# Kernel tuning notes

Measured on AMD Instinct MI355X. Metric: run time of the kernel, lower is better.

The kernel has to match this reference:

```python
import jax, jax.numpy as jnp
import numpy as np
from jax import lax

D_MODEL = 1024
N_HEADS = 8
D_HEAD = 64
D_INNER = N_HEADS * D_HEAD  # 512
B, T = 4, 4096
LN_EPS = 1e-5
NORM_EPS = 1e-12  # F.normalize default eps


def setup_inputs() -> dict:
    key = jax.random.key(0)
    ks = jax.random.split(key, 6)
    s_proj = (2.0 / (D_MODEL + D_INNER)) ** 0.5  # xavier_uniform-ish std
    x = jax.random.normal(ks[0], (B, T, D_MODEL), jnp.float32)
    Wq = jax.random.normal(ks[1], (D_MODEL, D_INNER), jnp.float32) * s_proj
    Wk = jax.random.normal(ks[2], (D_MODEL, D_INNER), jnp.float32) * s_proj
    Wv = jax.random.normal(ks[3], (D_MODEL, D_INNER), jnp.float32) * s_proj
    Wa = jax.random.normal(ks[4], (D_MODEL, D_INNER), jnp.float32) * s_proj
    ba = jnp.full((D_INNER,), 3.0, jnp.float32)  # nn.init.constant_(W_alpha.bias, 3.0)
    Wo = jax.random.normal(ks[5], (D_INNER, D_MODEL), jnp.float32) * s_proj
    gamma = jnp.ones((D_MODEL,), jnp.float32)
    beta = jnp.zeros((D_MODEL,), jnp.float32)
    return {"x": x, "Wq": Wq, "Wk": Wk, "Wv": Wv, "Wa": Wa, "ba": ba,
            "Wo": Wo, "gamma": gamma, "beta": beta}


def reference(x, Wq, Wk, Wv, Wa, ba, Wo, gamma, beta):
    Bx, Tx, _ = x.shape
    residual = x
    # LayerNorm
    mu = jnp.mean(x, axis=-1, keepdims=True)
    var = jnp.var(x, axis=-1, keepdims=True)
    xn = (x - mu) / jnp.sqrt(var + LN_EPS) * gamma + beta
    # Projections -> (B, T, H, d) -> time-major (T, B, H, d) for scan
    def heads(y):
        return jnp.moveaxis(y.reshape(Bx, Tx, N_HEADS, D_HEAD), 1, 0)
    q = heads(xn @ Wq)
    k = heads(xn @ Wk)
    v = heads(xn @ Wv)
    alpha = jax.nn.sigmoid(heads(xn @ Wa + ba))
    # F.normalize(k, dim=-1)
    knorm = jnp.linalg.norm(k, axis=-1, keepdims=True)
    k = k / jnp.maximum(knorm, NORM_EPS)

    # Recurrence: S_t = diag(a_t) S_{t-1} + k_t v_t^T ; o_t = S_t^T q_t
    def step(S, inp):
        q_t, k_t, v_t, a_t = inp  # each (B, H, d)
        S = a_t[..., None] * S + k_t[..., None] * v_t[..., None, :]  # (B,H,dk,dv)
        o_t = jnp.einsum('bhji,bhj->bhi', S, q_t)
        return S, o_t

    S0 = jnp.zeros((Bx, N_HEADS, D_HEAD, D_HEAD), x.dtype)
    _, outs = lax.scan(step, S0, (q, k, v, alpha))  # outs: (T, B, H, d)
    out = jnp.moveaxis(outs, 0, 1).reshape(Bx, Tx, D_INNER) @ Wo
    return out + residual
```

## Files before the change

### kernel.cpp

```cpp
#include <hip/hip_runtime.h>
#include <stdint.h>

#define NTOK   16384
#define DM     1024
#define DI     512
#define NH     8
#define DH     64
#define CHUNK  64
#define NCH    64
#define NBHC   2048

using short8 = __attribute__((ext_vector_type(8))) short;
using f32x4  = __attribute__((ext_vector_type(4))) float;

__device__ __forceinline__ unsigned short f2bf(float f) {
  union { float f; unsigned int u; } x; x.f = f;
  unsigned int u = x.u;
  return (unsigned short)((u + 0x7fffu + ((u >> 16) & 1u)) >> 16);
}
__device__ __forceinline__ float bf2f(unsigned short h) {
  union { unsigned int u; float f; } x; x.u = ((unsigned int)h) << 16; return x.f;
}

typedef const __attribute__((address_space(1))) void* gp1_t;
typedef __attribute__((address_space(3))) void* lp3_t;
__device__ __forceinline__ void gload_lds16(const void* g, void* l) {
  __builtin_amdgcn_global_load_lds((gp1_t)g, (lp3_t)l, 16, 0, 0);
}

__global__ __launch_bounds__(256) void init_kernel(const float* __restrict__ x,
                                                   const float* __restrict__ gamma,
                                                   const float* __restrict__ beta,
                                                   const float* __restrict__ Wq,
                                                   const float* __restrict__ Wk,
                                                   const float* __restrict__ Wv,
                                                   const float* __restrict__ Wa,
                                                   const float* __restrict__ Wo,
                                                   unsigned short* __restrict__ xn,
                                                   unsigned short* __restrict__ Wt,
                                                   unsigned short* __restrict__ Wot) {
  const int blk = blockIdx.x, tid = threadIdx.x;
  __shared__ float tile[32][33];
  __shared__ float rs_[4], rss_[4];
  if (blk < NTOK) {
    const int row = blk;
    float4 v = ((const float4*)(x + (long)row * DM))[tid];
    float s  = v.x + v.y + v.z + v.w;
    float ss = v.x * v.x + v.y * v.y + v.z * v.z + v.w * v.w;
    #pragma unroll
    for (int off = 32; off > 0; off >>= 1) { s += __shfl_down(s, off); ss += __shfl_down(ss, off); }
    int wave = tid >> 6, lane = tid & 63;
    if (lane == 0) { rs_[wave] = s; rss_[wave] = ss; }
    __syncthreads();
    s  = rs_[0] + rs_[1] + rs_[2] + rs_[3];
    ss = rss_[0] + rss_[1] + rss_[2] + rss_[3];
    float mu   = s * (1.f / DM);
    float var  = ss * (1.f / DM) - mu * mu;
    float rstd = rsqrtf(var + 1e-5f);
    int idx = tid * 4;
    float xv[4] = {v.x, v.y, v.z, v.w};
    unsigned short o[4];
    #pragma unroll
    for (int j = 0; j < 4; ++j) o[j] = f2bf((xv[j] - mu) * rstd * gamma[idx + j] + beta[idx + j]);
    uint2 pk; pk.x = (unsigned)o[0] | ((unsigned)o[1] << 16); pk.y = (unsigned)o[2] | ((unsigned)o[3] << 16);
    *(uint2*)(xn + (long)row * DM + idx) = pk;
  } else if (blk < NTOK + 2048) {
    const int id = blk - NTOK;
    const int z = id >> 9, r9 = id & 511;
    const float* in = (z == 0) ? Wq : (z == 1) ? Wk : (z == 2) ? Wv : Wa;
    unsigned short* o = Wt + (size_t)z * 512 * 1024;
    int bx = (r9 & 15) * 32, by = (r9 >> 4) * 32;
    int tx = tid & 31, ty = tid >> 5;
    #pragma unroll
    for (int r = ty; r < 32; r += 8) tile[r][tx] = in[(long)(by + r) * 512 + bx + tx];
    __syncthreads();
    #pragma unroll
    for (int r = ty; r < 32; r += 8) o[(long)(bx + r) * 1024 + by + tx] = f2bf(tile[tx][r]);
  } else {
    const int id = blk - NTOK - 2048;
    int bx = (id & 31) * 32, by = (id >> 5) * 32;
    int tx = tid & 31, ty = tid >> 5;
    #pragma unroll
    for (int r = ty; r < 32; r += 8) tile[r][tx] = Wo[(long)(by + r) * 1024 + bx + tx];
    __syncthreads();
    #pragma unroll
    for (int r = ty; r < 32; r += 8) Wot[(long)(bx + r) * 512 + by + tx] = f2bf(tile[tx][r]);
  }
}

#define EPSW 264
#define G4_TILE(T_, DOSTAGE_, WAITC_)                                         \
  {                                                                           \
    if (DOSTAGE_) {                                                           \
      const int s_ = (T_) + 3;                                                \
      unsigned short* sb_ = &sm[(s_ & 3) * 16384];                            \
      const long ko_ = (long)s_ * 32;                                         \
      gload_lds16(a0p + ko_, sb_ + dst);                                      \
      gload_lds16(a1p + ko_, sb_ + 4096 + dst);                               \
      gload_lds16(b0p + ko_, sb_ + 8192 + dst);                               \
      gload_lds16(b1p + ko_, sb_ + 12288 + dst);                              \
    }                                                                         \
    const unsigned short* cb_ = &sm[((T_) & 3) * 16384];                      \
    short8 av_[8], bv_[4];                                                    \
    _Pragma("unroll")                                                         \
    for (int mt = 0; mt < 8; ++mt) av_[mt] = *(const short8*)&cb_[aoff + mt * 512]; \
    _Pragma("unroll")                                                         \
    for (int nt = 0; nt < 4; ++nt) bv_[nt] = *(const short8*)&cb_[boff + nt * 512]; \
    __builtin_amdgcn_s_setprio(1);                                            \
    _Pragma("unroll")                                                         \
    for (int mt = 0; mt < 8; ++mt)                                            \
      _Pragma("unroll")                                                       \
      for (int nt = 0; nt < 4; ++nt)                                          \
        acc[mt][nt] = __builtin_amdgcn_mfma_f32_16x16x32_bf16(av_[mt], bv_[nt], acc[mt][nt], 0, 0, 0); \
    __builtin_amdgcn_s_setprio(0);                                            \
    asm volatile("s_waitcnt " WAITC_ ::: "memory");                           \
    __builtin_amdgcn_s_barrier();                                             \
    __builtin_amdgcn_sched_barrier(0);                                        \
  }

template <int MODE>
__global__ __launch_bounds__(512, 2) void gemm4s(const unsigned short* __restrict__ A,
                                                 const unsigned short* __restrict__ Bt,
                                                 unsigned short* __restrict__ Cb,
                                                 float* __restrict__ Cf,
                                                 const float* __restrict__ resid,
                                                 int M, int N, int K) {
  __shared__ __align__(16) unsigned short sm[65536];
  const int tid = threadIdx.x;
  const int wave = tid >> 6, lane = tid & 63;
  const int quad = lane >> 4, l16 = lane & 15;
  const int wm = wave >> 2, wn = wave & 3;

  const int nwg = gridDim.x;
  const int cpx = nwg >> 3;
  const int bid = blockIdx.x;
  const int swz = (bid & 7) * cpx + (bid >> 3);
  const int m0 = (swz & 63) * 256;
  const int n0 = (swz >> 6) * 256;

  const int r2 = tid >> 2;
  const int scol = ((tid & 3) * 8) ^ (((tid >> 3) & 3) * 8);
  const unsigned short* a0p = A + (long)(m0 + r2) * K + scol;
  const unsigned short* a1p = A + (long)(m0 + 128 + r2) * K + scol;
  const unsigned short* b0p = Bt + (long)(n0 + r2) * K + scol;
  const unsigned short* b1p = Bt + (long)(n0 + 128 + r2) * K + scol;
  const int dst = tid * 8;

  const int swzr = (quad * 8) ^ (((l16 >> 1) & 3) * 8);
  const int aoff = (wm * 128 + l16) * 32 + swzr;
  const int boff = 8192 + (wn * 64 + l16) * 32 + swzr;

  f32x4 acc[8][4];
  #pragma unroll
  for (int i = 0; i < 8; ++i)
    #pragma unroll
    for (int j = 0; j < 4; ++j) acc[i][j] = (f32x4){0.f, 0.f, 0.f, 0.f};

  const int NT = K >> 5;

  #pragma unroll
  for (int s = 0; s < 3; ++s) {
    unsigned short* sb = &sm[s * 16384];
    const long ko = (long)s * 32;
    gload_lds16(a0p + ko, sb + dst);
    gload_lds16(a1p + ko, sb + 4096 + dst);
    gload_lds16(b0p + ko, sb + 8192 + dst);
    gload_lds16(b1p + ko, sb + 12288 + dst);
  }
  asm volatile("s_waitcnt vmcnt(8)" ::: "memory");
  __builtin_amdgcn_s_barrier();
  __builtin_amdgcn_sched_barrier(0);

  int t = 0;
  for (; t < NT - 3; ++t) G4_TILE(t, true, "vmcnt(8)");
  G4_TILE(t, false, "vmcnt(4)"); ++t;
  G4_TILE(t, false, "vmcnt(0)"); ++t;
  G4_TILE(t, false, "vmcnt(0)");

  unsigned short* epi = sm;
  #pragma unroll
  for (int h = 0; h < 2; ++h) {
    if (wm == h) {
      #pragma unroll
      for (int fm = 0; fm < 8; ++fm)
        #pragma unroll
        for (int fn = 0; fn < 4; ++fn)
          #pragma unroll
          for (int r = 0; r < 4; ++r)
            epi[(fm * 16 + quad * 4 + r) * EPSW + wn * 64 + fn * 16 + l16] = f2bf(acc[fm][fn][r]);
    }
    __syncthreads();
    if (MODE == 0) {
      #pragma unroll
      for (int i = tid; i < 4096; i += 512) {
        int row = i >> 5, cc = (i & 31) * 8;
        uint4 v = *(const uint4*)&epi[row * EPSW + cc];
        *(uint4*)&Cb[(long)(m0 + h * 128 + row) * N + n0 + cc] = v;
      }
    } else {
      #pragma unroll
      for (int i = tid; i < 8192; i += 512) {
        int row = i >> 6, cc = (i & 63) * 4;
        long g = (long)(m0 + h * 128 + row) * N + n0 + cc;
        float4 rv = *(const float4*)&resid[g];
        uint2 pv = *(const uint2*)&epi[row * EPSW + cc];
        float4 ov;
        ov.x = bf2f((unsigned short)(pv.x & 0xffffu)) + rv.x;
        ov.y = bf2f((unsigned short)(pv.x >> 16))     + rv.y;
        ov.z = bf2f((unsigned short)(pv.y & 0xffffu)) + rv.z;
        ov.w = bf2f((unsigned short)(pv.y >> 16))     + rv.w;
        *(float4*)&Cf[g] = ov;
      }
    }
    __syncthreads();
  }
}

#define TS 72
__global__ __launch_bounds__(256) void prep_intra_kernel(const unsigned short* __restrict__ Cb,
                                                         const float* __restrict__ ba,
                                                         unsigned short* __restrict__ qt,
                                                         float* __restrict__ Dvec,
                                                         unsigned short* __restrict__ Ointra,
                                                         unsigned short* __restrict__ Tt) {
  const int bhc = blockIdx.x;
  const int c = bhc & 63, bh = bhc >> 6;
  const int h = bh & 7, b = bh >> 3;
  const int tid = threadIdx.x;
  __shared__ __align__(16) unsigned short Qb[4096], Kb[4096], Vb[4096], lamB[4096];
  __shared__ __align__(16) unsigned short Vt[64 * TS], Kt[64 * TS];
  __shared__ float rnF[64], lendF[64];
  const long rowbase = ((long)(b * 4096 + c * 64)) * 2048;
  const int hoff = h * 64;

  if (tid < 64) rnF[tid] = 0.f;
  __syncthreads();

  #pragma unroll
  for (int chunk = 0; chunk < 2; ++chunk) {
    int u = chunk * 256 + tid;
    int t = u >> 3, p = u & 7;
    long g = rowbase + (long)t * 2048 + hoff + p * 8;
    uint4 q4 = *(const uint4*)(Cb + g);
    uint4 k4 = *(const uint4*)(Cb + g + 512);
    uint4 v4 = *(const uint4*)(Cb + g + 1024);
    uint4 a4 = *(const uint4*)(Cb + g + 1536);
    *(uint4*)&Qb[u * 8] = q4;
    *(uint4*)&Kb[u * 8] = k4;
    *(uint4*)&Vb[u * 8] = v4;
    const unsigned short* as_ = (const unsigned short*)&a4;
    unsigned short al[8];
    #pragma unroll
    for (int j = 0; j < 8; ++j) {
      float z = bf2f(as_[j]) + ba[hoff + p * 8 + j];
      al[j] = f2bf(1.f / (1.f + __expf(-z)));
    }
    uint4 pa;
    pa.x = (unsigned)al[0] | ((unsigned)al[1] << 16); pa.y = (unsigned)al[2] | ((unsigned)al[3] << 16);
    pa.z = (unsigned)al[4] | ((unsigned)al[5] << 16); pa.w = (unsigned)al[6] | ((unsigned)al[7] << 16);
    *(uint4*)&lamB[u * 8] = pa;
    const unsigned short* ks = (const unsigned short*)&k4;
    float ssq = 0.f;
    #pragma unroll
    for (int j = 0; j < 8; ++j) { float kv = bf2f(ks[j]); ssq += kv * kv; }
    atomicAdd(&rnF[t], ssq);
  }
  __syncthreads();

  if (tid < 64) {
    int d = tid; float cum = 1.f;
    #pragma unroll
    for (int t = 0; t < 64; ++t) {
      cum *= bf2f(lamB[t * 64 + d]);
      lamB[t * 64 + d] = f2bf(cum);
    }
    Dvec[(long)bhc * 64 + d] = cum;
    lendF[d] = cum;
  } else if (tid < 128) {
    int t = tid - 64;
    rnF[t] = 1.f / fmaxf(sqrtf(rnF[t]), 1e-12f);
  }
  __syncthreads();

  #pragma unroll
  for (int j = 0; j < 16; ++j) {
    int e = j * 256 + tid;
    int t = e >> 6;
    float lam = bf2f(lamB[e]);
    float kn = bf2f(Kb[e]) * rnF[t];
    Qb[e] = f2bf(bf2f(Qb[e]) * lam);
    Kb[e] = f2bf(kn / lam);
  }
  __syncthreads();

  {
    const long obase = (long)bhc * 4096;
    uint4* gq = (uint4*)(qt + obase);
    const uint4* lq = (const uint4*)Qb;
    gq[tid] = lq[tid]; gq[tid + 256] = lq[tid + 256];
  }

  const long base = (long)bhc * 4096;
  const int wave = tid >> 6, lane = tid & 63, quad = lane >> 4, l16 = lane & 15;
  const int mrow = wave * 16 + l16;
  unsigned short* Ps = lamB;

  union { short8 v; short s[8]; } aI;
  aI.v = (short8){0,0,0,0,0,0,0,0};
  {
    int target = ((wave & 1) * 16 + l16) - quad * 8;
    if (target >= 0 && target < 8) aI.s[target] = (short)0x3F80;
  }
  const int bsel = (wave >> 1) * 32;

  {
    short8 a0 = *(const short8*)&Qb[mrow * 64 + quad * 8];
    short8 a1 = *(const short8*)&Qb[mrow * 64 + 32 + quad * 8];
    #pragma unroll
    for (int nt = 0; nt < 4; ++nt) {
      short8 b0 = *(const short8*)&Kb[(nt * 16 + l16) * 64 + quad * 8];
      short8 b1 = *(const short8*)&Kb[(nt * 16 + l16) * 64 + 32 + quad * 8];
      f32x4 acc = (f32x4){0.f, 0.f, 0.f, 0.f};
      acc = __builtin_amdgcn_mfma_f32_16x16x32_bf16(a0, b0, acc, 0, 0, 0);
      acc = __builtin_amdgcn_mfma_f32_16x16x32_bf16(a1, b1, acc, 0, 0, 0);
      #pragma unroll
      for (int r = 0; r < 4; ++r) {
        int t = wave * 16 + quad * 4 + r, u = nt * 16 + l16;
        Ps[t * 64 + u] = (u <= t) ? f2bf(acc[r]) : (unsigned short)0;
      }
    }
  }
  #pragma unroll
  for (int nt = 0; nt < 4; ++nt) {
    short8 bv = *(const short8*)&Vb[(nt * 16 + l16) * 64 + bsel + quad * 8];
    short8 bk = *(const short8*)&Kb[(nt * 16 + l16) * 64 + bsel + quad * 8];
    f32x4 av = (f32x4){0.f, 0.f, 0.f, 0.f};
    f32x4 ak = (f32x4){0.f, 0.f, 0.f, 0.f};
    av = __builtin_amdgcn_mfma_f32_16x16x32_bf16(aI.v, bv, av, 0, 0, 0);
    ak = __builtin_amdgcn_mfma_f32_16x16x32_bf16(aI.v, bk, ak, 0, 0, 0);
    #pragma unroll
    for (int r = 0; r < 4; ++r) {
      int i = wave * 16 + quad * 4 + r, t = nt * 16 + l16;
      Vt[i * TS + t] = f2bf(av[r]);
      Kt[i * TS + t] = f2bf(ak[r]);
    }
  }
  __syncthreads();

  {
    short8 a0 = *(const short8*)&Ps[mrow * 64 + quad * 8];
    short8 a1 = *(const short8*)&Ps[mrow * 64 + 32 + quad * 8];
    #pragma unroll
    for (int nt = 0; nt < 4; ++nt) {
      short8 b0 = *(const short8*)&Vt[(nt * 16 + l16) * TS + quad * 8];
      short8 b1 = *(const short8*)&Vt[(nt * 16 + l16) * TS + 32 + quad * 8];
      f32x4 acc = (f32x4){0.f, 0.f, 0.f, 0.f};
      acc = __builtin_amdgcn_mfma_f32_16x16x32_bf16(a0, b0, acc, 0, 0, 0);
      acc = __builtin_amdgcn_mfma_f32_16x16x32_bf16(a1, b1, acc, 0, 0, 0);
      #pragma unroll
      for (int r = 0; r < 4; ++r) {
        int t = wave * 16 + quad * 4 + r, i = nt * 16 + l16;
        Ointra[base + t * 64 + i] = f2bf(acc[r]);
      }
    }
  }
  {
    short8 a0 = *(const short8*)&Vt[mrow * TS + quad * 8];
    short8 a1 = *(const short8*)&Vt[mrow * TS + 32 + quad * 8];
    #pragma unroll
    for (int nt = 0; nt < 4; ++nt) {
      short8 b0 = *(const short8*)&Kt[(nt * 16 + l16) * TS + quad * 8];
      short8 b1 = *(const short8*)&Kt[(nt * 16 + l16) * TS + 32 + quad * 8];
      f32x4 acc = (f32x4){0.f, 0.f, 0.f, 0.f};
      acc = __builtin_amdgcn_mfma_f32_16x16x32_bf16(a0, b0, acc, 0, 0, 0);
      acc = __builtin_amdgcn_mfma_f32_16x16x32_bf16(a1, b1, acc, 0, 0, 0);
      float le = lendF[nt * 16 + l16];
      #pragma unroll
      for (int r = 0; r < 4; ++r) {
        int i = wave * 16 + quad * 4 + r, j = nt * 16 + l16;
        Tt[base + i * 64 + j] = f2bf(acc[r] * le);
      }
    }
  }
}

__global__ __launch_bounds__(256) void scan_kernel(const unsigned short* __restrict__ Tt,
                                                   const float* __restrict__ Dvec,
                                                   unsigned short* __restrict__ Sst) {
  const int bh = blockIdx.x;
  const int e = blockIdx.y * 256 + threadIdx.x;
  const int j = e & 63;
  float S = 0.f;
  for (int c = 0; c < 64; ++c) {
    const long idx = ((long)(bh * 64 + c)) * 4096 + e;
    const float dj = Dvec[((long)(bh * 64 + c)) * 64 + j];
    Sst[idx] = f2bf(S);
    S = dj * S + bf2f(Tt[idx]);
  }
}

__global__ __launch_bounds__(256) void combine_kernel(const unsigned short* __restrict__ qt,
                                                      const unsigned short* __restrict__ Sst,
                                                      const unsigned short* __restrict__ Ointra,
                                                      unsigned short* __restrict__ O) {
  const int bhc = blockIdx.x;
  const int c = bhc & 63, bh = bhc >> 6;
  const int h = bh & 7, b = bh >> 3;
  const long base = (long)bhc * 4096;
  __shared__ __align__(16) unsigned short Qs[4096], Sb[4096];
  const int tid = threadIdx.x;
  {
    const uint4* gq = (const uint4*)(qt + base);  uint4* lq = (uint4*)Qs;
    const uint4* gs = (const uint4*)(Sst + base); uint4* ls = (uint4*)Sb;
    lq[tid] = gq[tid]; lq[tid + 256] = gq[tid + 256];
    ls[tid] = gs[tid]; ls[tid + 256] = gs[tid + 256];
  }
  __syncthreads();
  const int wave = tid >> 6, lane = tid & 63, quad = lane >> 4, l16 = lane & 15;
  const int mrow = wave * 16 + l16;
  short8 a0 = *(const short8*)&Qs[mrow * 64 + quad * 8];
  short8 a1 = *(const short8*)&Qs[mrow * 64 + 32 + quad * 8];
  #pragma unroll
  for (int nt = 0; nt < 4; ++nt) {
    f32x4 acc;
    #pragma unroll
    for (int r = 0; r < 4; ++r) {
      int t = wave * 16 + quad * 4 + r, i = nt * 16 + l16;
      acc[r] = bf2f(Ointra[base + t * 64 + i]);
    }
    short8 b0 = *(const short8*)&Sb[(nt * 16 + l16) * 64 + quad * 8];
    short8 b1 = *(const short8*)&Sb[(nt * 16 + l16) * 64 + 32 + quad * 8];
    acc = __builtin_amdgcn_mfma_f32_16x16x32_bf16(a0, b0, acc, 0, 0, 0);
    acc = __builtin_amdgcn_mfma_f32_16x16x32_bf16(a1, b1, acc, 0, 0, 0);
    #pragma unroll
    for (int r = 0; r < 4; ++r) {
      int t = wave * 16 + quad * 4 + r, i = nt * 16 + l16;
      O[((long)(b * 4096 + c * 64 + t)) * 512 + h * 64 + i] = f2bf(acc[r]);
    }
  }
}

extern "C" void kernel_launch(void* const* d_in, const int* in_sizes, int n_in,
                              void* d_out, int out_size, void* d_ws, size_t ws_size,
                              hipStream_t stream) {
  const float* x     = (const float*)d_in[0];
  const float* Wq    = (const float*)d_in[1];
  const float* Wk    = (const float*)d_in[2];
  const float* Wv    = (const float*)d_in[3];
  const float* Wa    = (const float*)d_in[4];
  const float* ba    = (const float*)d_in[5];
  const float* Wo    = (const float*)d_in[6];
  const float* gamma = (const float*)d_in[7];
  const float* beta  = (const float*)d_in[8];
  float* out = (float*)d_out;

  char* ws = (char*)d_ws;
  const size_t KB = 1024;
  unsigned short* Wt     = (unsigned short*)(ws + 0 * KB);
  unsigned short* Wot    = (unsigned short*)(ws + 4096 * KB);
  float*          Dvec   = (float*)         (ws + 5120 * KB);
  unsigned short* qt     = (unsigned short*)(ws + 5632 * KB);
  unsigned short* Ttb    = (unsigned short*)(ws + 22016 * KB);
  unsigned short* Sst    = (unsigned short*)(ws + 38400 * KB);
  unsigned short* xn     = (unsigned short*)(ws + 54784 * KB);
  unsigned short* Ointra = (unsigned short*)(ws + 54784 * KB);
  unsigned short* Ob     = (unsigned short*)(ws + 71168 * KB);
  unsigned short* Cb     = (unsigned short*)(ws + 87552 * KB);

  init_kernel<<<NTOK + 2048 + 512, 256, 0, stream>>>(x, gamma, beta, Wq, Wk, Wv, Wa, Wo, xn, Wt, Wot);
  gemm4s<0><<<512, 512, 0, stream>>>(xn, Wt, Cb, nullptr, nullptr, NTOK, 2048, 1024);
  prep_intra_kernel<<<NBHC, 256, 0, stream>>>(Cb, ba, qt, Dvec, Ointra, Ttb);
  scan_kernel<<<dim3(32, 16), 256, 0, stream>>>(Ttb, Dvec, Sst);
  combine_kernel<<<NBHC, 256, 0, stream>>>(qt, Sst, Ointra, Ob);
  gemm4s<1><<<256, 512, 0, stream>>>(Ob, Wot, nullptr, out, x, NTOK, 1024, 512);
}
```

Before: 312.9 us.

## Use smaller-tile output GEMM and stage intra-chunk stores through LDS

Splits the templated GEMM in two. The output projection now uses a 128x128 tile, 256-thread kernel with 1024 workgroups instead of 256 workgroups of 256x256, so more CUs get work for the smaller N=1024, K=512 problem. The prep and combine kernels now stage the Ointra and Tt tiles in shared memory and write or read them with coalesced 16-byte global accesses instead of scattered 2-byte ones. The trade-off is more per-tile load overhead and lower reuse in the output GEMM, plus extra LDS traffic and one more barrier in prep.

Result: no change. 312.4 us (-0.2%).

```diff
diff --git a/kernel.cpp b/kernel.cpp
--- a/kernel.cpp
+++ b/kernel.cpp
@@ -118,12 +118,9 @@
     __builtin_amdgcn_sched_barrier(0);                                        \
   }
 
-template <int MODE>
-__global__ __launch_bounds__(512, 2) void gemm4s(const unsigned short* __restrict__ A,
+__global__ __launch_bounds__(512, 2) void gemm1k(const unsigned short* __restrict__ A,
                                                  const unsigned short* __restrict__ Bt,
                                                  unsigned short* __restrict__ Cb,
-                                                 float* __restrict__ Cf,
-                                                 const float* __restrict__ resid,
                                                  int M, int N, int K) {
   __shared__ __align__(16) unsigned short sm[65536];
   const int tid = threadIdx.x;
@@ -190,29 +187,123 @@
             epi[(fm * 16 + quad * 4 + r) * EPSW + wn * 64 + fn * 16 + l16] = f2bf(acc[fm][fn][r]);
     }
     __syncthreads();
-    if (MODE == 0) {
+    #pragma unroll
+    for (int i = tid; i < 4096; i += 512) {
+      int row = i >> 5, cc = (i & 31) * 8;
+      uint4 v = *(const uint4*)&epi[row * EPSW + cc];
+      *(uint4*)&Cb[(long)(m0 + h * 128 + row) * N + n0 + cc] = v;
+    }
+    __syncthreads();
+  }
+}
+
+__global__ __launch_bounds__(256, 2) void gemm2k(const unsigned short* __restrict__ A,
+                                                 const unsigned short* __restrict__ Bt,
+                                                 float* __restrict__ Cf,
+                                                 const float* __restrict__ resid,
+                                                 int M, int N, int K) {
+  __shared__ __align__(16) unsigned short sm[32768];
+  const int tid = threadIdx.x;
+  const int wave = tid >> 6, lane = tid & 63;
+  const int quad = lane >> 4, l16 = lane & 15;
+  const int wm = wave >> 1, wn = wave & 1;
+
+  const int nwg = gridDim.x;
+  const int cpx = nwg >> 3;
+  const int bid = blockIdx.x;
+  const int swz = (bid & 7) * cpx + (bid >> 3);
+  const int m0 = (swz & 127) * 128;
+  const int n0 = (swz >> 7) * 128;
+
+  const int r2 = tid >> 2;
+  const int scol = ((tid & 3) * 8) ^ (((tid >> 3) & 3) * 8);
+  const unsigned short* a0p = A + (long)(m0 + r2) * K + scol;
+  const unsigned short* a1p = A + (long)(m0 + 64 + r2) * K + scol;
+  const unsigned short* b0p = Bt + (long)(n0 + r2) * K + scol;
+  const unsigned short* b1p = Bt + (long)(n0 + 64 + r2) * K + scol;
+  const int dst = tid * 8;
+
+  const int swzr = (quad * 8) ^ (((l16 >> 1) & 3) * 8);
+  const int aoff = wm * 2048 + l16 * 32 + swzr;
+  const int boff = 4096 + wn * 2048 + l16 * 32 + swzr;
+
+  f32x4 acc[4][4];
+  #pragma unroll
+  for (int i = 0; i < 4; ++i)
+    #pragma unroll
+    for (int j = 0; j < 4; ++j) acc[i][j] = (f32x4){0.f, 0.f, 0.f, 0.f};
+
+  const int NT = K >> 5;
+
+  #pragma unroll
+  for (int s = 0; s < 3; ++s) {
+    unsigned short* sb = &sm[s * 8192];
+    const long ko = (long)s * 32;
+    gload_lds16(a0p + ko, sb + dst);
+    gload_lds16(a1p + ko, sb + 2048 + dst);
+    gload_lds16(b0p + ko, sb + 4096 + dst);
+    gload_lds16(b1p + ko, sb + 6144 + dst);
+  }
+  asm volatile("s_waitcnt vmcnt(8)" ::: "memory");
+  __builtin_amdgcn_s_barrier();
+  __builtin_amdgcn_sched_barrier(0);
+
+#define G2_TILE(T_, DOSTAGE_, WAITC_)                                         \
+  {                                                                           \
+    if (DOSTAGE_) {                                                           \
+      const int s_ = (T_) + 3;                                                \
+      unsigned short* sb_ = &sm[(s_ & 3) * 8192];                             \
+      const long ko_ = (long)s_ * 32;                                         \
+      gload_lds16(a0p + ko_, sb_ + dst);                                      \
+      gload_lds16(a1p + ko_, sb_ + 2048 + dst);                               \
+      gload_lds16(b0p + ko_, sb_ + 4096 + dst);                               \
+      gload_lds16(b1p + ko_, sb_ + 6144 + dst);                               \
+    }                                                                         \
+    const unsigned short* cb_ = &sm[((T_) & 3) * 8192];                       \
+    short8 av_[4], bv_[4];                                                    \
+    _Pragma("unroll")                                                         \
+    for (int mt = 0; mt < 4; ++mt) av_[mt] = *(const short8*)&cb_[aoff + mt * 512]; \
+    _Pragma("unroll")                                                         \
+    for (int nt = 0; nt < 4; ++nt) bv_[nt] = *(const short8*)&cb_[boff + nt * 512]; \
+    __builtin_amdgcn_s_setprio(1);                                            \
+    _Pragma("unroll")                                                         \
+    for (int mt = 0; mt < 4; ++mt)                                            \
+      _Pragma("unroll")                                                       \
+      for (int nt = 0; nt < 4; ++nt)                                          \
+        acc[mt][nt] = __builtin_amdgcn_mfma_f32_16x16x32_bf16(av_[mt], bv_[nt], acc[mt][nt], 0, 0, 0); \
+    __builtin_amdgcn_s_setprio(0);                                            \
+    asm volatile("s_waitcnt " WAITC_ ::: "memory");                           \
+    __builtin_amdgcn_s_barrier();                                             \
+    __builtin_amdgcn_sched_barrier(0);                                        \
+  }
+
+  int t = 0;
+  for (; t < NT - 3; ++t) G2_TILE(t, true, "vmcnt(8)");
+  G2_TILE(t, false, "vmcnt(4)"); ++t;
+  G2_TILE(t, false, "vmcnt(0)"); ++t;
+  G2_TILE(t, false, "vmcnt(0)");
+
+  unsigned short* epi = sm;
+  #pragma unroll
+  for (int mt = 0; mt < 4; ++mt)
+    #pragma unroll
+    for (int nt = 0; nt < 4; ++nt)
       #pragma unroll
-      for (int i = tid; i < 4096; i += 512) {
-        int row = i >> 5, cc = (i & 31) * 8;
-        uint4 v = *(const uint4*)&epi[row * EPSW + cc];
-        *(uint4*)&Cb[(long)(m0 + h * 128 + row) * N + n0 + cc] = v;
-      }
-    } else {
-      #pragma unroll
-      for (int i = tid; i < 8192; i += 512) {
-        int row = i >> 6, cc = (i & 63) * 4;
-        long g = (long)(m0 + h * 128 + row) * N + n0 + cc;
-        float4 rv = *(const float4*)&resid[g];
-        uint2 pv = *(const uint2*)&epi[row * EPSW + cc];
-        float4 ov;
-        ov.x = bf2f((unsigned short)(pv.x & 0xffffu)) + rv.x;
-        ov.y = bf2f((unsigned short)(pv.x >> 16))     + rv.y;
-        ov.z = bf2f((unsigned short)(pv.y & 0xffffu)) + rv.z;
-        ov.w = bf2f((unsigned short)(pv.y >> 16))     + rv.w;
-        *(float4*)&Cf[g] = ov;
-      }
-    }
-    __syncthreads();
+      for (int r = 0; r < 4; ++r)
+        epi[(wm * 64 + mt * 16 + quad * 4 + r) * 136 + wn * 64 + nt * 16 + l16] = f2bf(acc[mt][nt][r]);
+  __syncthreads();
+  #pragma unroll
+  for (int i = tid; i < 4096; i += 256) {
+    int row = i >> 5, cc = (i & 31) * 4;
+    long g = (long)(m0 + row) * N + n0 + cc;
+    float4 rv = *(const float4*)&resid[g];
+    uint2 pv = *(const uint2*)&epi[row * 136 + cc];
+    float4 ov;
+    ov.x = bf2f((unsigned short)(pv.x & 0xffffu)) + rv.x;
+    ov.y = bf2f((unsigned short)(pv.x >> 16))     + rv.y;
+    ov.z = bf2f((unsigned short)(pv.y & 0xffffu)) + rv.z;
+    ov.w = bf2f((unsigned short)(pv.y >> 16))     + rv.w;
+    *(float4*)&Cf[g] = ov;
   }
 }
 
@@ -360,7 +451,7 @@
       #pragma unroll
       for (int r = 0; r < 4; ++r) {
         int t = wave * 16 + quad * 4 + r, i = nt * 16 + l16;
-        Ointra[base + t * 64 + i] = f2bf(acc[r]);
+        Vb[t * 64 + i] = f2bf(acc[r]);
       }
     }
   }
@@ -378,9 +469,16 @@
       #pragma unroll
       for (int r = 0; r < 4; ++r) {
         int i = wave * 16 + quad * 4 + r, j = nt * 16 + l16;
-        Tt[base + i * 64 + j] = f2bf(acc[r] * le);
+        Kb[i * 64 + j] = f2bf(acc[r] * le);
       }
     }
+  }
+  __syncthreads();
+  {
+    const uint4* ov = (const uint4*)Vb; uint4* og = (uint4*)(Ointra + base);
+    const uint4* tv = (const uint4*)Kb; uint4* tg = (uint4*)(Tt + base);
+    og[tid] = ov[tid]; og[tid + 256] = ov[tid + 256];
+    tg[tid] = tv[tid]; tg[tid + 256] = tv[tid + 256];
   }
 }
 
@@ -407,13 +505,15 @@
   const int c = bhc & 63, bh = bhc >> 6;
   const int h = bh & 7, b = bh >> 3;
   const long base = (long)bhc * 4096;
-  __shared__ __align__(16) unsigned short Qs[4096], Sb[4096];
+  __shared__ __align__(16) unsigned short Qs[4096], Sb[4096], Os[4096];
   const int tid = threadIdx.x;
   {
-    const uint4* gq = (const uint4*)(qt + base);  uint4* lq = (uint4*)Qs;
-    const uint4* gs = (const uint4*)(Sst + base); uint4* ls = (uint4*)Sb;
+    const uint4* gq = (const uint4*)(qt + base);     uint4* lq = (uint4*)Qs;
+    const uint4* gs = (const uint4*)(Sst + base);    uint4* ls = (uint4*)Sb;
+    const uint4* go = (const uint4*)(Ointra + base); uint4* lo = (uint4*)Os;
     lq[tid] = gq[tid]; lq[tid + 256] = gq[tid + 256];
     ls[tid] = gs[tid]; ls[tid + 256] = gs[tid + 256];
+    lo[tid] = go[tid]; lo[tid + 256] = go[tid + 256];
   }
   __syncthreads();
   const int wave = tid >> 6, lane = tid & 63, quad = lane >> 4, l16 = lane & 15;
@@ -426,7 +526,7 @@
     #pragma unroll
     for (int r = 0; r < 4; ++r) {
       int t = wave * 16 + quad * 4 + r, i = nt * 16 + l16;
-      acc[r] = bf2f(Ointra[base + t * 64 + i]);
+      acc[r] = bf2f(Os[t * 64 + i]);
     }
     short8 b0 = *(const short8*)&Sb[(nt * 16 + l16) * 64 + quad * 8];
     short8 b1 = *(const short8*)&Sb[(nt * 16 + l16) * 64 + 32 + quad * 8];
@@ -468,9 +568,9 @@
   unsigned short* Cb     = (unsigned short*)(ws + 87552 * KB);
 
   init_kernel<<<NTOK + 2048 + 512, 256, 0, stream>>>(x, gamma, beta, Wq, Wk, Wv, Wa, Wo, xn, Wt, Wot);
-  gemm4s<0><<<512, 512, 0, stream>>>(xn, Wt, Cb, nullptr, nullptr, NTOK, 2048, 1024);
+  gemm1k<<<512, 512, 0, stream>>>(xn, Wt, Cb, NTOK, 2048, 1024);
   prep_intra_kernel<<<NBHC, 256, 0, stream>>>(Cb, ba, qt, Dvec, Ointra, Ttb);
   scan_kernel<<<dim3(32, 16), 256, 0, stream>>>(Ttb, Dvec, Sst);
   combine_kernel<<<NBHC, 256, 0, stream>>>(qt, Sst, Ointra, Ob);
-  gemm4s<1><<<256, 512, 0, stream>>>(Ob, Wot, nullptr, out, x, NTOK, 1024, 512);
-}
+  gemm2k<<<1024, 256, 0, stream>>>(Ob, Wot, out, x, NTOK, 1024, 512);
+}
```
